# Kernel optimization log

Measured on AMD Instinct MI355X. Metric: run time of the kernel, lower is better.

The kernel has to match this reference:

```python
import jax, jax.numpy as jnp
import numpy as np

NPOINT, NSAMPLE, RADIUS = 2048, 32, 0.2
EPS = 1e-5


def setup_inputs() -> dict:
    key = jax.random.key(0)
    ks = jax.random.split(key, 12)
    B, N, C = 8, 8192, 64
    mlp = [64, 64, 128]
    inp = {
        "xyz": jax.random.normal(ks[0], (B, 3, N), dtype=jnp.float32),
        "points": jax.random.normal(ks[1], (B, C, N), dtype=jnp.float32),
    }
    last = C + 3  # use_xyz concatenates 3 relative coords
    for i, out in enumerate(mlp, 1):
        inp[f"W{i}"] = jax.random.normal(ks[2 * i], (out, last), dtype=jnp.float32) / np.sqrt(last).astype(np.float32)
        inp[f"b{i}"] = jnp.zeros((out,), jnp.float32)
        inp[f"g{i}"] = jnp.ones((out,), jnp.float32)
        inp[f"be{i}"] = jnp.zeros((out,), jnp.float32)
        last = out
    return inp


def fps(xyz_t, npoint):
    """Farthest point sampling. xyz_t: (B,N,3) -> (B,npoint) int32 indices."""
    xyz_t = jax.lax.stop_gradient(xyz_t)  # indices are non-differentiable
    B, N, _ = xyz_t.shape

    def step(carry, _):
        dists, far = carry  # (B,N), (B,)
        cent = jnp.take_along_axis(xyz_t, far[:, None, None], axis=1)  # (B,1,3)
        d = jnp.sum((xyz_t - cent) ** 2, axis=-1)
        dists = jnp.minimum(dists, d)
        nf = jnp.argmax(dists, axis=-1).astype(jnp.int32)
        return (dists, nf), far

    init = (jnp.full((B, N), 1e10, xyz_t.dtype), jnp.zeros((B,), jnp.int32))
    _, idxs = jax.lax.scan(step, init, None, length=npoint)
    return jnp.transpose(idxs)  # (B, npoint)


def ball_query(xyz_t, new_xyz_t, radius, nsample):
    """First-nsample-in-radius neighbor indices, padded with first hit.
    xyz_t (B,N,3), new_xyz_t (B,M,3) -> (B,M,nsample) int32."""
    B, N, _ = xyz_t.shape
    # squared distances via gemm to avoid (B,M,N,3) intermediate
    sq = (jnp.sum(new_xyz_t ** 2, -1)[:, :, None]
          + jnp.sum(xyz_t ** 2, -1)[:, None, :]
          - 2.0 * jnp.einsum('bmd,bnd->bmn', new_xyz_t, xyz_t))  # (B,M,N)
    cand = jnp.where(sq < radius * radius, jnp.arange(N, dtype=jnp.int32), N)
    idx = jnp.sort(cand, axis=-1)[:, :, :nsample]  # first k in-radius by index order
    first = idx[:, :, :1]
    first = jnp.where(first == N, 0, first)  # guard empty groups
    idx = jnp.where(idx == N, first, idx)
    return idx


def group(feat, idx):
    """feat (B,C,N), idx (B,M,k) -> (B,C,M,k) gathered neighbor features."""
    return jnp.take_along_axis(feat[:, :, None, :], idx[:, None, :, :], axis=3)


def conv_bn_relu(x, W, b, g, be):
    """Shared 1x1 Conv2d + BatchNorm2d (batch stats, training mode) + ReLU.
    x: (B,C,M,K) -> (B,O,M,K)."""
    y = jnp.einsum('oc,bcmk->bomk', W, x) + b[None, :, None, None]
    mu = jnp.mean(y, axis=(0, 2, 3), keepdims=True)
    var = jnp.var(y, axis=(0, 2, 3), keepdims=True)
    y = (y - mu) * jax.lax.rsqrt(var + EPS)
    y = y * g[None, :, None, None] + be[None, :, None, None]
    return jax.nn.relu(y)


def reference(xyz, points, W1, b1, g1, be1, W2, b2, g2, be2, W3, b3, g3, be3):
    xyz_t = jnp.transpose(xyz, (0, 2, 1))  # (B,N,3)
    fidx = fps(xyz_t, NPOINT)  # (B,M)
    new_xyz = jnp.take_along_axis(xyz, fidx[:, None, :], axis=2)  # (B,3,M)
    idx = ball_query(xyz_t, jnp.transpose(new_xyz, (0, 2, 1)), RADIUS, NSAMPLE)  # (B,M,K)
    grouped_xyz = group(xyz, idx) - new_xyz[:, :, :, None]  # (B,3,M,K) centered
    grouped_pts = group(points, idx)  # (B,f,M,K)
    x = jnp.concatenate([grouped_xyz, grouped_pts], axis=1)  # (B,f+3,M,K)
    x = conv_bn_relu(x, W1, b1, g1, be1)
    x = conv_bn_relu(x, W2, b2, g2, be2)
    x = conv_bn_relu(x, W3, b3, g3, be3)
    new_points = jnp.max(x, axis=3)  # (B,mlp[-1],M)
    return (new_xyz, new_points)
```

## Files before the change

### kernel.cpp

```cpp
#include <hip/hip_runtime.h>

#define BB 8
#define NN 8192
#define MM 2048
#define KK 32
#define NTOT (BB*MM*KK)

#define WS_PTS_T  0
#define WS_XYZN   4194304
#define WS_IDX    5242880
#define WS_GPART  5767168
#define WS_PARAMS 6291456
#define WS_ZMAX   6292480
#define WS_ZMIN   8389632
#define WS_TOTAL  10486784

typedef float v2f __attribute__((ext_vector_type(2)));

__global__ __launch_bounds__(256) void k_transpose(const float* __restrict__ pts,
                                                   float* __restrict__ pts_t){
  __shared__ float tile[64][65];
  int bid = blockIdx.x;
  int b = bid >> 7;
  int n0 = (bid & 127) << 6;
  int tx = threadIdx.x & 63, ty = threadIdx.x >> 6;
  const float* src = pts + (size_t)b*64*NN;
  #pragma unroll
  for (int c = ty; c < 64; c += 4)
    tile[c][tx] = src[(size_t)c*NN + n0 + tx];
  __syncthreads();
  float* dst = pts_t + ((size_t)b*NN + n0)*64;
  #pragma unroll
  for (int r = ty; r < 64; r += 4)
    dst[(size_t)r*64 + tx] = tile[tx][r];
}

__global__ __launch_bounds__(256) void k_xyzn(const float* __restrict__ xyz,
                                              float4* __restrict__ xyzn){
  #pragma clang fp contract(off)
  int i = blockIdx.x*256 + threadIdx.x;
  int b = i >> 13, n = i & 8191;
  const float* p = xyz + (size_t)b*3*NN;
  float x = p[n], y = p[NN+n], z = p[2*NN+n];
  float nrm = (x*x + y*y) + z*z;
  xyzn[i] = make_float4(x, y, z, nrm);
}

#define FPS_DPP_STEP(ctrl, rmask)                                            \
  {                                                                          \
    unsigned int lo_ = (unsigned int)key, hi_ = (unsigned int)(key >> 32);   \
    unsigned int sl_ = (unsigned int)__builtin_amdgcn_update_dpp(            \
        (int)lo_, (int)lo_, (ctrl), (rmask), 0xf, false);                    \
    unsigned int sh_ = (unsigned int)__builtin_amdgcn_update_dpp(            \
        (int)hi_, (int)hi_, (ctrl), (rmask), 0xf, false);                    \
    unsigned long long ok_ = ((unsigned long long)sh_ << 32) | sl_;          \
    if (ok_ > key) key = ok_;                                                \
  }

__global__ __launch_bounds__(512,1) void k_fps(const float* __restrict__ xyz,
                                               float* __restrict__ out_newxyz){
  #pragma clang fp contract(off)
  __shared__ float4 sp4[NN];
  __shared__ unsigned long long swk[2][8];
  int b = blockIdx.x, tid = threadIdx.x;
  const float* xb = xyz + (size_t)b*3*NN;
  int n0 = tid << 4;
  v2f px[8], py[8], pz[8], dd[8];
  const float4* xb4 = (const float4*)xb;
  #pragma unroll
  for (int q = 0; q < 4; ++q){
    float4 X = xb4[(n0>>2) + q];
    float4 Y = xb4[(NN>>2) + (n0>>2) + q];
    float4 Z = xb4[((2*NN)>>2) + (n0>>2) + q];
    px[2*q]   = (v2f){X.x, X.y}; px[2*q+1] = (v2f){X.z, X.w};
    py[2*q]   = (v2f){Y.x, Y.y}; py[2*q+1] = (v2f){Y.z, Y.w};
    pz[2*q]   = (v2f){Z.x, Z.y}; pz[2*q+1] = (v2f){Z.z, Z.w};
    dd[2*q]   = (v2f){1e10f,1e10f}; dd[2*q+1] = (v2f){1e10f,1e10f};
    sp4[n0+4*q+0] = make_float4(X.x, Y.x, Z.x, 0.f);
    sp4[n0+4*q+1] = make_float4(X.y, Y.y, Z.y, 0.f);
    sp4[n0+4*q+2] = make_float4(X.z, Y.z, Z.z, 0.f);
    sp4[n0+4*q+3] = make_float4(X.w, Y.w, Z.w, 0.f);
  }
  __syncthreads();
  float4 c0 = sp4[0];
  float cx = c0.x, cy = c0.y, cz = c0.z;
  float* ob = out_newxyz + (size_t)b*3*MM;
  int lane = tid & 63, wid = tid >> 6;
  for (int t = 0; t < MM; ++t){
    if (tid == 0){ ob[t] = cx; ob[MM+t] = cy; ob[2*MM+t] = cz; }
    v2f cvx = (v2f){cx,cx}, cvy = (v2f){cy,cy}, cvz = (v2f){cz,cz};
    v2f bv2 = (v2f){-1.f,-1.f};
    #pragma unroll
    for (int g = 0; g < 8; ++g){
      v2f dx = px[g]-cvx, dy = py[g]-cvy, dz = pz[g]-cvz;
      v2f xx = dx*dx, yy = dy*dy, zz = dz*dz;
      v2f s = xx + yy;
      v2f d = s + zz;
      v2f nd = __builtin_elementwise_min(dd[g], d);
      dd[g] = nd;
      bv2 = __builtin_elementwise_max(bv2, nd);
    }
    float bv = fmaxf(bv2.x, bv2.y);
    int bj = 0;
    #pragma unroll
    for (int g = 7; g >= 0; --g){
      if (dd[g].y == bv) bj = 2*g+1;
      if (dd[g].x == bv) bj = 2*g;
    }
    unsigned int n = (unsigned int)(n0 + bj);
    unsigned long long key =
        ((unsigned long long)__float_as_uint(bv) << 32) | (unsigned int)(~n);
    FPS_DPP_STEP(0x111, 0xf)
    FPS_DPP_STEP(0x112, 0xf)
    FPS_DPP_STEP(0x114, 0xf)
    FPS_DPP_STEP(0x118, 0xf)
    FPS_DPP_STEP(0x142, 0xa)
    FPS_DPP_STEP(0x143, 0xc)
    int buf = t & 1;
    if (lane == 63) swk[buf][wid] = key;
    __syncthreads();
    const unsigned long long* kk = swk[buf];
    unsigned long long k0=kk[0], k1=kk[1], k2=kk[2], k3=kk[3];
    unsigned long long k4=kk[4], k5=kk[5], k6=kk[6], k7=kk[7];
    unsigned long long a = (k0>k1)?k0:k1, c = (k2>k3)?k2:k3;
    unsigned long long e = (k4>k5)?k4:k5, f = (k6>k7)?k6:k7;
    unsigned long long g2 = (a>c)?a:c,   h2 = (e>f)?e:f;
    unsigned long long kmax = (g2>h2)?g2:h2;
    int far = (int)(~(unsigned int)kmax) & (NN-1);
    float4 c4 = sp4[far];
    cx = c4.x; cy = c4.y; cz = c4.z;
  }
}

__global__ __launch_bounds__(256) void k_ballq(const float4* __restrict__ xyzn,
                                               const float* __restrict__ newxyz,
                                               int* __restrict__ idx){
  #pragma clang fp contract(off)
  __shared__ unsigned long long s_mask[32][129];
  __shared__ float4 s_c4[32];
  const float R2 = (float)(0.2*0.2);
  int b = blockIdx.x >> 6;
  int m0 = (blockIdx.x & 63) << 5;
  int tid = threadIdx.x, lane = tid & 63, wv = tid >> 6;
  const float* nb = newxyz + (size_t)b*3*MM;
  if (tid < 32){
    int m = m0 + tid;
    float cx = nb[m], cy = nb[MM+m], cz = nb[2*MM+m];
    float cn = (cx*cx + cy*cy) + cz*cz;
    s_c4[tid] = make_float4(cx, cy, cz, cn);
  }
  __syncthreads();
  const float4* src = xyzn + (size_t)b*NN;
  for (int ci = 0; ci < 32; ++ci){
    int ch = ci*4 + wv;
    float4 p = src[ch*64 + lane];
    #pragma unroll 8
    for (int mi = 0; mi < 32; ++mi){
      float4 c = s_c4[mi];
      float dot = (c.x*p.x + c.y*p.y) + c.z*p.z;
      float sq = (c.w + p.w) - 2.0f*dot;
      unsigned long long mk = __ballot(sq < R2);
      if (lane == 0) s_mask[mi][ch] = mk;
    }
  }
  __syncthreads();
  if (tid < 32){
    int m = m0 + tid;
    int* om = idx + ((size_t)(b*MM + m))*KK;
    int filled = 0, first = -1;
    for (int ch = 0; ch < 128 && filled < KK; ++ch){
      unsigned long long mk = s_mask[tid][ch];
      while (mk){
        int bp = __builtin_ctzll(mk);
        mk &= mk - 1;
        int j = ch*64 + bp;
        if (first < 0) first = j;
        om[filled++] = j;
        if (filled == KK) break;
      }
    }
    int pad = (first < 0) ? 0 : first;
    for (int s = filled; s < KK; ++s) om[s] = pad;
  }
}

__device__ __forceinline__ void accum_ch(float4* acc, const float4* w4, int c, float v){
  #pragma unroll
  for (int o4 = 0; o4 < 16; ++o4){
    float4 w = w4[c*16 + o4];
    acc[o4].x = fmaf(w.x, v, acc[o4].x);
    acc[o4].y = fmaf(w.y, v, acc[o4].y);
    acc[o4].z = fmaf(w.z, v, acc[o4].z);
    acc[o4].w = fmaf(w.w, v, acc[o4].w);
  }
}

__device__ __forceinline__ void conv1_pos(float4* acc, const float* s_w1,
    const float* pts_t, const float4* xyzn, const float* nb, int b, int m, int j){
  #pragma unroll
  for (int o4 = 0; o4 < 16; ++o4) acc[o4] = make_float4(0.f,0.f,0.f,0.f);
  float4 P = xyzn[(size_t)b*NN + j];
  float x0 = P.x - nb[m], x1 = P.y - nb[MM+m], x2 = P.z - nb[2*MM+m];
  const float4* w4 = (const float4*)s_w1;
  accum_ch(acc, w4, 0, x0);
  accum_ch(acc, w4, 1, x1);
  accum_ch(acc, w4, 2, x2);
  const float4* pf = (const float4*)(pts_t + ((size_t)b*NN + j)*64);
  #pragma unroll
  for (int c4 = 0; c4 < 16; ++c4){
    float4 v = pf[c4];
    accum_ch(acc, w4, 3+4*c4+0, v.x);
    accum_ch(acc, w4, 3+4*c4+1, v.y);
    accum_ch(acc, w4, 3+4*c4+2, v.z);
    accum_ch(acc, w4, 3+4*c4+3, v.w);
  }
}

__global__ __launch_bounds__(256,1) void k_conv1_stats(const float* __restrict__ pts_t,
    const float4* __restrict__ xyzn, const float* __restrict__ newxyz,
    const int* __restrict__ idx, const float* __restrict__ W1, float* __restrict__ gpart){
  __shared__ float s_w1[67*64];
  __shared__ float s_z[256*68];
  __shared__ float s_part[4*64*2];
  int tid = threadIdx.x;
  for (int i = tid; i < 67*64; i += 256){ int c = i>>6, o = i&63; s_w1[i] = W1[o*67 + c]; }
  __syncthreads();
  int bid = blockIdx.x, b = bid >> 8, m0 = (bid & 255) << 3;
  int m = m0 + (tid >> 5), k = tid & 31;
  int j = idx[((size_t)(b*MM + m))*KK + k];
  const float* nb = newxyz + (size_t)b*3*MM;
  float4 acc[16];
  conv1_pos(acc, s_w1, pts_t, xyzn, nb, b, m, j);
  #pragma unroll
  for (int o4 = 0; o4 < 16; ++o4) *(float4*)&s_z[tid*68 + o4*4] = acc[o4];
  __syncthreads();
  int o = tid & 63, q = tid >> 6;
  float s = 0.f, sq = 0.f;
  for (int p = q*64; p < q*64 + 64; ++p){ float v = s_z[p*68 + o]; s += v; sq = fmaf(v, v, sq); }
  s_part[(q*64+o)*2] = s; s_part[(q*64+o)*2+1] = sq;
  __syncthreads();
  if (tid < 64){
    float S = 0.f, SQ = 0.f;
    #pragma unroll
    for (int qq = 0; qq < 4; ++qq){ S += s_part[(qq*64+tid)*2]; SQ += s_part[(qq*64+tid)*2+1]; }
    gpart[(size_t)tid*2048 + bid] = S;
    gpart[(size_t)(128+tid)*2048 + bid] = SQ;
  }
}

__global__ __launch_bounds__(256) void k_bnfin(const float* __restrict__ gpart,
    const float* __restrict__ g, const float* __restrict__ be, float* __restrict__ params){
  int o = blockIdx.x, t = threadIdx.x;
  double s = 0.0, sq = 0.0;
  for (int i = t; i < 2048; i += 256){
    s  += (double)gpart[(size_t)o*2048 + i];
    sq += (double)gpart[(size_t)(128+o)*2048 + i];
  }
  __shared__ double ds[256], dq[256];
  ds[t] = s; dq[t] = sq; __syncthreads();
  for (int off = 128; off > 0; off >>= 1){
    if (t < off){ ds[t] += ds[t+off]; dq[t] += dq[t+off]; }
    __syncthreads();
  }
  if (t == 0){
    double mu = ds[0] / (double)NTOT;
    double var = dq[0] / (double)NTOT - mu*mu;
    float A = g[o] / sqrtf((float)var + 1e-5f);
    float Cc = be[o] - (float)mu * A;
    params[o] = A; params[128+o] = Cc;
  }
}

__global__ __launch_bounds__(256,1) void k_conv2_stats(const float* __restrict__ pts_t,
    const float4* __restrict__ xyzn, const float* __restrict__ newxyz,
    const int* __restrict__ idx, const float* __restrict__ W1, const float* __restrict__ W2,
    const float* __restrict__ params1, float* __restrict__ gpart){
  __shared__ float s_w1[67*64];
  __shared__ float s_w2[64*64];
  __shared__ float s_p[128];
  __shared__ float s_z[256*68];
  __shared__ float s_part[4*64*2];
  int tid = threadIdx.x;
  for (int i = tid; i < 67*64; i += 256){ int c = i>>6, o = i&63; s_w1[i] = W1[o*67 + c]; }
  for (int i = tid; i < 64*64; i += 256){ int c = i>>6, o = i&63; s_w2[i] = W2[o*64 + c]; }
  if (tid < 64){ s_p[tid] = params1[tid]; s_p[64+tid] = params1[128+tid]; }
  __syncthreads();
  int bid = blockIdx.x, b = bid >> 8, m0 = (bid & 255) << 3;
  int m = m0 + (tid >> 5), k = tid & 31;
  int j = idx[((size_t)(b*MM + m))*KK + k];
  const float* nb = newxyz + (size_t)b*3*MM;
  float4 acc[16];
  conv1_pos(acc, s_w1, pts_t, xyzn, nb, b, m, j);
  float4 h[16];
  #pragma unroll
  for (int o4 = 0; o4 < 16; ++o4){
    float4 z = acc[o4], hh;
    hh.x = fmaxf(fmaf(s_p[4*o4+0], z.x, s_p[64+4*o4+0]), 0.f);
    hh.y = fmaxf(fmaf(s_p[4*o4+1], z.y, s_p[64+4*o4+1]), 0.f);
    hh.z = fmaxf(fmaf(s_p[4*o4+2], z.z, s_p[64+4*o4+2]), 0.f);
    hh.w = fmaxf(fmaf(s_p[4*o4+3], z.w, s_p[64+4*o4+3]), 0.f);
    h[o4] = hh;
  }
  float4 a2[16];
  #pragma unroll
  for (int o4 = 0; o4 < 16; ++o4) a2[o4] = make_float4(0.f,0.f,0.f,0.f);
  const float4* w24 = (const float4*)s_w2;
  #pragma unroll
  for (int c4 = 0; c4 < 16; ++c4){
    accum_ch(a2, w24, 4*c4+0, h[c4].x);
    accum_ch(a2, w24, 4*c4+1, h[c4].y);
    accum_ch(a2, w24, 4*c4+2, h[c4].z);
    accum_ch(a2, w24, 4*c4+3, h[c4].w);
  }
  #pragma unroll
  for (int o4 = 0; o4 < 16; ++o4) *(float4*)&s_z[tid*68 + o4*4] = a2[o4];
  __syncthreads();
  int o = tid & 63, q = tid >> 6;
  float s = 0.f, sq = 0.f;
  for (int p = q*64; p < q*64 + 64; ++p){ float v = s_z[p*68 + o]; s += v; sq = fmaf(v, v, sq); }
  s_part[(q*64+o)*2] = s; s_part[(q*64+o)*2+1] = sq;
  __syncthreads();
  if (tid < 64){
    float S = 0.f, SQ = 0.f;
    #pragma unroll
    for (int qq = 0; qq < 4; ++qq){ S += s_part[(qq*64+tid)*2]; SQ += s_part[(qq*64+tid)*2+1]; }
    gpart[(size_t)tid*2048 + bid] = S;
    gpart[(size_t)(128+tid)*2048 + bid] = SQ;
  }
}

__global__ __launch_bounds__(256,1) void k_conv3(const float* __restrict__ pts_t,
    const float4* __restrict__ xyzn, const float* __restrict__ newxyz,
    const int* __restrict__ idx, const float* __restrict__ W1, const float* __restrict__ W2,
    const float* __restrict__ W3, const float* __restrict__ params1,
    const float* __restrict__ params2, float* __restrict__ gpart,
    float* __restrict__ zmax, float* __restrict__ zmin){
  __shared__ float s_w1[67*64];
  __shared__ float s_w2[64*64];
  __shared__ float s_p[256];
  __shared__ float s_z[256*68];
  __shared__ float s_sm[8*128*2];
  int tid = threadIdx.x;
  for (int i = tid; i < 67*64; i += 256){ int c = i>>6, o = i&63; s_w1[i] = W1[o*67 + c]; }
  for (int i = tid; i < 64*64; i += 256){ int c = i>>6, o = i&63; s_w2[i] = W2[o*64 + c]; }
  if (tid < 64){
    s_p[tid]      = params1[tid];     s_p[64+tid]  = params1[128+tid];
    s_p[128+tid]  = params2[tid];     s_p[192+tid] = params2[128+tid];
  }
  __syncthreads();
  int bid = blockIdx.x, b = bid >> 8, m0 = (bid & 255) << 3;
  {
    int m = m0 + (tid >> 5), k = tid & 31;
    int j = idx[((size_t)(b*MM + m))*KK + k];
    const float* nb = newxyz + (size_t)b*3*MM;
    float4 acc[16];
    conv1_pos(acc, s_w1, pts_t, xyzn, nb, b, m, j);
    float4 h[16];
    #pragma unroll
    for (int o4 = 0; o4 < 16; ++o4){
      float4 z = acc[o4], hh;
      hh.x = fmaxf(fmaf(s_p[4*o4+0], z.x, s_p[64+4*o4+0]), 0.f);
      hh.y = fmaxf(fmaf(s_p[4*o4+1], z.y, s_p[64+4*o4+1]), 0.f);
      hh.z = fmaxf(fmaf(s_p[4*o4+2], z.z, s_p[64+4*o4+2]), 0.f);
      hh.w = fmaxf(fmaf(s_p[4*o4+3], z.w, s_p[64+4*o4+3]), 0.f);
      h[o4] = hh;
    }
    float4 a2[16];
    #pragma unroll
    for (int o4 = 0; o4 < 16; ++o4) a2[o4] = make_float4(0.f,0.f,0.f,0.f);
    const float4* w24 = (const float4*)s_w2;
    #pragma unroll
    for (int c4 = 0; c4 < 16; ++c4){
      accum_ch(a2, w24, 4*c4+0, h[c4].x);
      accum_ch(a2, w24, 4*c4+1, h[c4].y);
      accum_ch(a2, w24, 4*c4+2, h[c4].z);
      accum_ch(a2, w24, 4*c4+3, h[c4].w);
    }
    #pragma unroll
    for (int o4 = 0; o4 < 16; ++o4){
      float4 z = a2[o4], hh;
      hh.x = fmaxf(fmaf(s_p[128+4*o4+0], z.x, s_p[192+4*o4+0]), 0.f);
      hh.y = fmaxf(fmaf(s_p[128+4*o4+1], z.y, s_p[192+4*o4+1]), 0.f);
      hh.z = fmaxf(fmaf(s_p[128+4*o4+2], z.z, s_p[192+4*o4+2]), 0.f);
      hh.w = fmaxf(fmaf(s_p[128+4*o4+3], z.w, s_p[192+4*o4+3]), 0.f);
      *(float4*)&s_z[tid*68 + o4*4] = hh;
    }
  }
  __syncthreads();
  int ml = tid >> 5, og = tid & 31;
  float accK[4][32];
  #pragma unroll
  for (int oo = 0; oo < 4; ++oo)
    #pragma unroll
    for (int k2 = 0; k2 < 32; ++k2) accK[oo][k2] = 0.f;
  const float4* w3g = (const float4*)W3;
  #pragma unroll
  for (int c4 = 0; c4 < 16; ++c4){
    float4 w[4];
    #pragma unroll
    for (int oo = 0; oo < 4; ++oo) w[oo] = w3g[(og*4+oo)*16 + c4];
    #pragma unroll
    for (int k2 = 0; k2 < 32; ++k2){
      float4 hv = *(const float4*)&s_z[(ml*32+k2)*68 + c4*4];
      #pragma unroll
      for (int oo = 0; oo < 4; ++oo){
        accK[oo][k2] = fmaf(w[oo].x, hv.x, accK[oo][k2]);
        accK[oo][k2] = fmaf(w[oo].y, hv.y, accK[oo][k2]);
        accK[oo][k2] = fmaf(w[oo].z, hv.z, accK[oo][k2]);
        accK[oo][k2] = fmaf(w[oo].w, hv.w, accK[oo][k2]);
      }
    }
  }
  int m = m0 + ml;
  #pragma unroll
  for (int oo = 0; oo < 4; ++oo){
    float mx = -3.4e38f, mn = 3.4e38f, s = 0.f, sq = 0.f;
    #pragma unroll
    for (int k2 = 0; k2 < 32; ++k2){
      float v = accK[oo][k2];
      mx = fmaxf(mx, v); mn = fminf(mn, v);
      s += v; sq = fmaf(v, v, sq);
    }
    int o = og*4 + oo;
    zmax[((size_t)(b*128 + o))*MM + m] = mx;
    zmin[((size_t)(b*128 + o))*MM + m] = mn;
    s_sm[(ml*128+o)*2] = s; s_sm[(ml*128+o)*2+1] = sq;
  }
  __syncthreads();
  {
    int o = tid >> 1, st = tid & 1;
    float S = 0.f;
    #pragma unroll
    for (int mm = 0; mm < 8; ++mm) S += s_sm[(mm*128+o)*2 + st];
    gpart[(size_t)(st*128+o)*2048 + bid] = S;
  }
}

__global__ __launch_bounds__(256) void k_out(const float* __restrict__ zmax,
    const float* __restrict__ zmin, const float* __restrict__ params3,
    float* __restrict__ out){
  int i = blockIdx.x*256 + threadIdx.x;
  int o = (i >> 11) & 127;
  float A = params3[o], Cc = params3[128+o];
  float v = (A >= 0.f) ? fmaf(A, zmax[i], Cc) : fmaf(A, zmin[i], Cc);
  out[49152 + i] = fmaxf(v, 0.f);
}

extern "C" void kernel_launch(void* const* d_in, const int* in_sizes, int n_in,
                              void* d_out, int out_size, void* d_ws, size_t ws_size,
                              hipStream_t stream){
  const float* xyz    = (const float*)d_in[0];
  const float* points = (const float*)d_in[1];
  const float* W1  = (const float*)d_in[2];
  const float* g1  = (const float*)d_in[4];
  const float* be1 = (const float*)d_in[5];
  const float* W2  = (const float*)d_in[6];
  const float* g2  = (const float*)d_in[8];
  const float* be2 = (const float*)d_in[9];
  const float* W3  = (const float*)d_in[10];
  const float* g3  = (const float*)d_in[12];
  const float* be3 = (const float*)d_in[13];

  if (ws_size < (size_t)WS_TOTAL * sizeof(float)) return;

  float*  ws     = (float*)d_ws;
  float*  pts_t  = ws + WS_PTS_T;
  float4* xyzn   = (float4*)(ws + WS_XYZN);
  int*    idx    = (int*)(ws + WS_IDX);
  float*  gpart  = ws + WS_GPART;
  float*  params = ws + WS_PARAMS;
  float*  zmax   = ws + WS_ZMAX;
  float*  zmin   = ws + WS_ZMIN;
  float*  out    = (float*)d_out;
  float*  newxyz = out;

  hipLaunchKernelGGL(k_fps,       dim3(8),    dim3(512), 0, stream, xyz, newxyz);
  hipLaunchKernelGGL(k_transpose, dim3(1024), dim3(256), 0, stream, points, pts_t);
  hipLaunchKernelGGL(k_xyzn,      dim3(256),  dim3(256), 0, stream, xyz, xyzn);
  hipLaunchKernelGGL(k_ballq,     dim3(512),  dim3(256), 0, stream, xyzn, newxyz, idx);
  hipLaunchKernelGGL(k_conv1_stats, dim3(2048), dim3(256), 0, stream,
                     pts_t, xyzn, newxyz, idx, W1, gpart);
  hipLaunchKernelGGL(k_bnfin, dim3(64), dim3(256), 0, stream, gpart, g1, be1, params+0);
  hipLaunchKernelGGL(k_conv2_stats, dim3(2048), dim3(256), 0, stream,
                     pts_t, xyzn, newxyz, idx, W1, W2, params+0, gpart);
  hipLaunchKernelGGL(k_bnfin, dim3(64), dim3(256), 0, stream, gpart, g2, be2, params+256);
  hipLaunchKernelGGL(k_conv3, dim3(2048), dim3(256), 0, stream,
                     pts_t, xyzn, newxyz, idx, W1, W2, W3, params+0, params+256,
                     gpart, zmax, zmin);
  hipLaunchKernelGGL(k_bnfin, dim3(128), dim3(256), 0, stream, gpart, g3, be3, params+512);
  hipLaunchKernelGGL(k_out, dim3(8192), dim3(256), 0, stream, zmax, zmin, params+512, out);
}
```

Measured before the change: 3.087 ms.

## Register-tile conv1/conv2 stats kernels and batch FPS centroid output writes

```diff
diff --git a/kernel.cpp b/kernel.cpp
--- a/kernel.cpp
+++ b/kernel.cpp
@@ -86,49 +86,53 @@
   float cx = c0.x, cy = c0.y, cz = c0.z;
   float* ob = out_newxyz + (size_t)b*3*MM;
   int lane = tid & 63, wid = tid >> 6;
-  for (int t = 0; t < MM; ++t){
-    if (tid == 0){ ob[t] = cx; ob[MM+t] = cy; ob[2*MM+t] = cz; }
-    v2f cvx = (v2f){cx,cx}, cvy = (v2f){cy,cy}, cvz = (v2f){cz,cz};
-    v2f bv2 = (v2f){-1.f,-1.f};
-    #pragma unroll
-    for (int g = 0; g < 8; ++g){
-      v2f dx = px[g]-cvx, dy = py[g]-cvy, dz = pz[g]-cvz;
-      v2f xx = dx*dx, yy = dy*dy, zz = dz*dz;
-      v2f s = xx + yy;
-      v2f d = s + zz;
-      v2f nd = __builtin_elementwise_min(dd[g], d);
-      dd[g] = nd;
-      bv2 = __builtin_elementwise_max(bv2, nd);
-    }
-    float bv = fmaxf(bv2.x, bv2.y);
-    int bj = 0;
-    #pragma unroll
-    for (int g = 7; g >= 0; --g){
-      if (dd[g].y == bv) bj = 2*g+1;
-      if (dd[g].x == bv) bj = 2*g;
-    }
-    unsigned int n = (unsigned int)(n0 + bj);
-    unsigned long long key =
-        ((unsigned long long)__float_as_uint(bv) << 32) | (unsigned int)(~n);
-    FPS_DPP_STEP(0x111, 0xf)
-    FPS_DPP_STEP(0x112, 0xf)
-    FPS_DPP_STEP(0x114, 0xf)
-    FPS_DPP_STEP(0x118, 0xf)
-    FPS_DPP_STEP(0x142, 0xa)
-    FPS_DPP_STEP(0x143, 0xc)
-    int buf = t & 1;
-    if (lane == 63) swk[buf][wid] = key;
-    __syncthreads();
-    const unsigned long long* kk = swk[buf];
-    unsigned long long k0=kk[0], k1=kk[1], k2=kk[2], k3=kk[3];
-    unsigned long long k4=kk[4], k5=kk[5], k6=kk[6], k7=kk[7];
-    unsigned long long a = (k0>k1)?k0:k1, c = (k2>k3)?k2:k3;
-    unsigned long long e = (k4>k5)?k4:k5, f = (k6>k7)?k6:k7;
-    unsigned long long g2 = (a>c)?a:c,   h2 = (e>f)?e:f;
-    unsigned long long kmax = (g2>h2)?g2:h2;
-    int far = (int)(~(unsigned int)kmax) & (NN-1);
-    float4 c4 = sp4[far];
-    cx = c4.x; cy = c4.y; cz = c4.z;
+  for (int s = 0; s < 4; ++s){
+    float ox = 0.f, oy = 0.f, oz = 0.f;
+    for (int ti = 0; ti < 512; ++ti){
+      if (tid == ti){ ox = cx; oy = cy; oz = cz; }
+      v2f cvx = (v2f){cx,cx}, cvy = (v2f){cy,cy}, cvz = (v2f){cz,cz};
+      v2f bv2 = (v2f){-1.f,-1.f};
+      #pragma unroll
+      for (int g = 0; g < 8; ++g){
+        v2f dx = px[g]-cvx, dy = py[g]-cvy, dz = pz[g]-cvz;
+        v2f xx = dx*dx, yy = dy*dy, zz = dz*dz;
+        v2f sum = xx + yy;
+        v2f d = sum + zz;
+        v2f nd = __builtin_elementwise_min(dd[g], d);
+        dd[g] = nd;
+        bv2 = __builtin_elementwise_max(bv2, nd);
+      }
+      float bv = fmaxf(bv2.x, bv2.y);
+      int bj = 0;
+      #pragma unroll
+      for (int g = 7; g >= 0; --g){
+        if (dd[g].y == bv) bj = 2*g+1;
+        if (dd[g].x == bv) bj = 2*g;
+      }
+      unsigned int n = (unsigned int)(n0 + bj);
+      unsigned long long key =
+          ((unsigned long long)__float_as_uint(bv) << 32) | (unsigned int)(~n);
+      FPS_DPP_STEP(0x111, 0xf)
+      FPS_DPP_STEP(0x112, 0xf)
+      FPS_DPP_STEP(0x114, 0xf)
+      FPS_DPP_STEP(0x118, 0xf)
+      FPS_DPP_STEP(0x142, 0xa)
+      FPS_DPP_STEP(0x143, 0xc)
+      int buf = ti & 1;
+      if (lane == 63) swk[buf][wid] = key;
+      __syncthreads();
+      const unsigned long long* kk = swk[buf];
+      unsigned long long k0=kk[0], k1=kk[1], k2=kk[2], k3=kk[3];
+      unsigned long long k4=kk[4], k5=kk[5], k6=kk[6], k7=kk[7];
+      unsigned long long a = (k0>k1)?k0:k1, c = (k2>k3)?k2:k3;
+      unsigned long long e = (k4>k5)?k4:k5, f = (k6>k7)?k6:k7;
+      unsigned long long g2 = (a>c)?a:c,   h2 = (e>f)?e:f;
+      unsigned long long kmax = (g2>h2)?g2:h2;
+      int far = (int)(~(unsigned int)kmax) & (NN-1);
+      float4 c4 = sp4[far];
+      cx = c4.x; cy = c4.y; cz = c4.z;
+    }
+    ob[(s<<9)+tid] = ox; ob[MM+(s<<9)+tid] = oy; ob[2*MM+(s<<9)+tid] = oz;
   }
 }
 
@@ -184,6 +188,142 @@
   }
 }
 
+#define XST 260
+
+__device__ __forceinline__ void fma_po(float4& a0, float4& a1, float w,
+                                       const float4& xA, const float4& xB){
+  a0.x = fmaf(w, xA.x, a0.x); a0.y = fmaf(w, xA.y, a0.y);
+  a0.z = fmaf(w, xA.z, a0.z); a0.w = fmaf(w, xA.w, a0.w);
+  a1.x = fmaf(w, xB.x, a1.x); a1.y = fmaf(w, xB.y, a1.y);
+  a1.z = fmaf(w, xB.z, a1.z); a1.w = fmaf(w, xB.w, a1.w);
+}
+
+__device__ __forceinline__ void gemm_step(float4 (&acc)[8][2], const float* sw,
+                                          const float* sx, int c, int ob8, int pb){
+  float4 xA = *(const float4*)&sx[c*XST + pb];
+  float4 xB = *(const float4*)&sx[c*XST + pb + 4];
+  float4 wA = *(const float4*)&sw[c*64 + ob8];
+  float4 wB = *(const float4*)&sw[c*64 + ob8 + 4];
+  fma_po(acc[0][0], acc[0][1], wA.x, xA, xB);
+  fma_po(acc[1][0], acc[1][1], wA.y, xA, xB);
+  fma_po(acc[2][0], acc[2][1], wA.z, xA, xB);
+  fma_po(acc[3][0], acc[3][1], wA.w, xA, xB);
+  fma_po(acc[4][0], acc[4][1], wB.x, xA, xB);
+  fma_po(acc[5][0], acc[5][1], wB.y, xA, xB);
+  fma_po(acc[6][0], acc[6][1], wB.z, xA, xB);
+  fma_po(acc[7][0], acc[7][1], wB.w, xA, xB);
+}
+
+__device__ __forceinline__ void gather_col(float* sx, const float* pts_t,
+    const float4* xyzn, const float* nb, const int* idx, int b, int bid, int tid){
+  int m0 = (bid & 255) << 3;
+  int m = m0 + (tid >> 5), k = tid & 31;
+  int j = idx[((size_t)(b*MM + m))*KK + k];
+  float4 P = xyzn[(size_t)b*NN + j];
+  sx[0*XST + tid] = P.x - nb[m];
+  sx[1*XST + tid] = P.y - nb[MM+m];
+  sx[2*XST + tid] = P.z - nb[2*MM+m];
+  const float4* pf = (const float4*)(pts_t + ((size_t)b*NN + j)*64);
+  #pragma unroll
+  for (int c4 = 0; c4 < 16; ++c4){
+    float4 v = pf[c4];
+    sx[(3+4*c4+0)*XST + tid] = v.x;
+    sx[(3+4*c4+1)*XST + tid] = v.y;
+    sx[(3+4*c4+2)*XST + tid] = v.z;
+    sx[(3+4*c4+3)*XST + tid] = v.w;
+  }
+}
+
+__device__ __forceinline__ void tile_stats(const float4 (&acc)[8][2], float* s_pp,
+    float* gpart, int ob8, int pg, int tid, int bid, int nch_base){
+  #pragma unroll
+  for (int oi = 0; oi < 8; ++oi){
+    float4 a0 = acc[oi][0], a1 = acc[oi][1];
+    float s  = ((a0.x+a0.y)+(a0.z+a0.w)) + ((a1.x+a1.y)+(a1.z+a1.w));
+    float q2 = ((a0.x*a0.x + a0.y*a0.y) + (a0.z*a0.z + a0.w*a0.w))
+             + ((a1.x*a1.x + a1.y*a1.y) + (a1.z*a1.z + a1.w*a1.w));
+    int o = ob8 + oi;
+    s_pp[o*64 + pg*2 + 0] = s;
+    s_pp[o*64 + pg*2 + 1] = q2;
+  }
+  __syncthreads();
+  if (tid < 128){
+    int o = tid >> 1, st = tid & 1;
+    float S = 0.f;
+    #pragma unroll 8
+    for (int q = 0; q < 32; ++q) S += s_pp[o*64 + q*2 + st];
+    gpart[(size_t)(st*128 + nch_base + o)*2048 + bid] = S;
+  }
+}
+
+__global__ __launch_bounds__(256,1) void k_conv1_stats(const float* __restrict__ pts_t,
+    const float4* __restrict__ xyzn, const float* __restrict__ newxyz,
+    const int* __restrict__ idx, const float* __restrict__ W1, float* __restrict__ gpart){
+  __shared__ float s_w1[67*64];
+  __shared__ float s_x[67*XST];
+  int tid = threadIdx.x;
+  for (int i = tid; i < 67*64; i += 256){ int c = i>>6, o = i&63; s_w1[i] = W1[o*67 + c]; }
+  int bid = blockIdx.x, b = bid >> 8;
+  const float* nb = newxyz + (size_t)b*3*MM;
+  gather_col(s_x, pts_t, xyzn, nb, idx, b, bid, tid);
+  __syncthreads();
+  int oq = tid & 7, pg = tid >> 3;
+  int ob8 = oq*8, pb = pg*8;
+  float4 acc[8][2];
+  #pragma unroll
+  for (int oi=0;oi<8;++oi){ acc[oi][0]=make_float4(0,0,0,0); acc[oi][1]=make_float4(0,0,0,0); }
+  for (int c = 0; c < 67; ++c) gemm_step(acc, s_w1, s_x, c, ob8, pb);
+  __syncthreads();
+  tile_stats(acc, s_x, gpart, ob8, pg, tid, bid, 0);
+}
+
+__global__ __launch_bounds__(256,1) void k_conv2_stats(const float* __restrict__ pts_t,
+    const float4* __restrict__ xyzn, const float* __restrict__ newxyz,
+    const int* __restrict__ idx, const float* __restrict__ W1, const float* __restrict__ W2,
+    const float* __restrict__ params1, float* __restrict__ gpart){
+  __shared__ float s_w1[67*64];
+  __shared__ float s_w2[64*64];
+  __shared__ float s_p[128];
+  __shared__ float s_x[67*XST];
+  int tid = threadIdx.x;
+  for (int i = tid; i < 67*64; i += 256){ int c = i>>6, o = i&63; s_w1[i] = W1[o*67 + c]; }
+  for (int i = tid; i < 64*64; i += 256){ int c = i>>6, o = i&63; s_w2[i] = W2[o*64 + c]; }
+  if (tid < 64){ s_p[tid] = params1[tid]; s_p[64+tid] = params1[128+tid]; }
+  int bid = blockIdx.x, b = bid >> 8;
+  const float* nb = newxyz + (size_t)b*3*MM;
+  gather_col(s_x, pts_t, xyzn, nb, idx, b, bid, tid);
+  __syncthreads();
+  int oq = tid & 7, pg = tid >> 3;
+  int ob8 = oq*8, pb = pg*8;
+  float4 acc[8][2];
+  #pragma unroll
+  for (int oi=0;oi<8;++oi){ acc[oi][0]=make_float4(0,0,0,0); acc[oi][1]=make_float4(0,0,0,0); }
+  for (int c = 0; c < 67; ++c) gemm_step(acc, s_w1, s_x, c, ob8, pb);
+  float4 hreg[8][2];
+  #pragma unroll
+  for (int oi = 0; oi < 8; ++oi){
+    float A = s_p[ob8+oi], C = s_p[64+ob8+oi];
+    float4 z0 = acc[oi][0], z1 = acc[oi][1], h0, h1;
+    h0.x = fmaxf(fmaf(A, z0.x, C), 0.f); h0.y = fmaxf(fmaf(A, z0.y, C), 0.f);
+    h0.z = fmaxf(fmaf(A, z0.z, C), 0.f); h0.w = fmaxf(fmaf(A, z0.w, C), 0.f);
+    h1.x = fmaxf(fmaf(A, z1.x, C), 0.f); h1.y = fmaxf(fmaf(A, z1.y, C), 0.f);
+    h1.z = fmaxf(fmaf(A, z1.z, C), 0.f); h1.w = fmaxf(fmaf(A, z1.w, C), 0.f);
+    hreg[oi][0] = h0; hreg[oi][1] = h1;
+  }
+  __syncthreads();
+  #pragma unroll
+  for (int oi = 0; oi < 8; ++oi){
+    *(float4*)&s_x[(ob8+oi)*XST + pb]     = hreg[oi][0];
+    *(float4*)&s_x[(ob8+oi)*XST + pb + 4] = hreg[oi][1];
+  }
+  __syncthreads();
+  #pragma unroll
+  for (int oi=0;oi<8;++oi){ acc[oi][0]=make_float4(0,0,0,0); acc[oi][1]=make_float4(0,0,0,0); }
+  for (int c = 0; c < 64; ++c) gemm_step(acc, s_w2, s_x, c, ob8, pb);
+  __syncthreads();
+  tile_stats(acc, s_x, gpart, ob8, pg, tid, bid, 0);
+}
+
 __device__ __forceinline__ void accum_ch(float4* acc, const float4* w4, int c, float v){
   #pragma unroll
   for (int o4 = 0; o4 < 16; ++o4){
@@ -216,38 +356,6 @@
   }
 }
 
-__global__ __launch_bounds__(256,1) void k_conv1_stats(const float* __restrict__ pts_t,
-    const float4* __restrict__ xyzn, const float* __restrict__ newxyz,
-    const int* __restrict__ idx, const float* __restrict__ W1, float* __restrict__ gpart){
-  __shared__ float s_w1[67*64];
-  __shared__ float s_z[256*68];
-  __shared__ float s_part[4*64*2];
-  int tid = threadIdx.x;
-  for (int i = tid; i < 67*64; i += 256){ int c = i>>6, o = i&63; s_w1[i] = W1[o*67 + c]; }
-  __syncthreads();
-  int bid = blockIdx.x, b = bid >> 8, m0 = (bid & 255) << 3;
-  int m = m0 + (tid >> 5), k = tid & 31;
-  int j = idx[((size_t)(b*MM + m))*KK + k];
-  const float* nb = newxyz + (size_t)b*3*MM;
-  float4 acc[16];
-  conv1_pos(acc, s_w1, pts_t, xyzn, nb, b, m, j);
-  #pragma unroll
-  for (int o4 = 0; o4 < 16; ++o4) *(float4*)&s_z[tid*68 + o4*4] = acc[o4];
-  __syncthreads();
-  int o = tid & 63, q = tid >> 6;
-  float s = 0.f, sq = 0.f;
-  for (int p = q*64; p < q*64 + 64; ++p){ float v = s_z[p*68 + o]; s += v; sq = fmaf(v, v, sq); }
-  s_part[(q*64+o)*2] = s; s_part[(q*64+o)*2+1] = sq;
-  __syncthreads();
-  if (tid < 64){
-    float S = 0.f, SQ = 0.f;
-    #pragma unroll
-    for (int qq = 0; qq < 4; ++qq){ S += s_part[(qq*64+tid)*2]; SQ += s_part[(qq*64+tid)*2+1]; }
-    gpart[(size_t)tid*2048 + bid] = S;
-    gpart[(size_t)(128+tid)*2048 + bid] = SQ;
-  }
-}
-
 __global__ __launch_bounds__(256) void k_bnfin(const float* __restrict__ gpart,
     const float* __restrict__ g, const float* __restrict__ be, float* __restrict__ params){
   int o = blockIdx.x, t = threadIdx.x;
@@ -268,64 +376,6 @@
     float A = g[o] / sqrtf((float)var + 1e-5f);
     float Cc = be[o] - (float)mu * A;
     params[o] = A; params[128+o] = Cc;
-  }
-}
-
-__global__ __launch_bounds__(256,1) void k_conv2_stats(const float* __restrict__ pts_t,
-    const float4* __restrict__ xyzn, const float* __restrict__ newxyz,
-    const int* __restrict__ idx, const float* __restrict__ W1, const float* __restrict__ W2,
-    const float* __restrict__ params1, float* __restrict__ gpart){
-  __shared__ float s_w1[67*64];
-  __shared__ float s_w2[64*64];
-  __shared__ float s_p[128];
-  __shared__ float s_z[256*68];
-  __shared__ float s_part[4*64*2];
-  int tid = threadIdx.x;
-  for (int i = tid; i < 67*64; i += 256){ int c = i>>6, o = i&63; s_w1[i] = W1[o*67 + c]; }
-  for (int i = tid; i < 64*64; i += 256){ int c = i>>6, o = i&63; s_w2[i] = W2[o*64 + c]; }
-  if (tid < 64){ s_p[tid] = params1[tid]; s_p[64+tid] = params1[128+tid]; }
-  __syncthreads();
-  int bid = blockIdx.x, b = bid >> 8, m0 = (bid & 255) << 3;
-  int m = m0 + (tid >> 5), k = tid & 31;
-  int j = idx[((size_t)(b*MM + m))*KK + k];
-  const float* nb = newxyz + (size_t)b*3*MM;
-  float4 acc[16];
-  conv1_pos(acc, s_w1, pts_t, xyzn, nb, b, m, j);
-  float4 h[16];
-  #pragma unroll
-  for (int o4 = 0; o4 < 16; ++o4){
-    float4 z = acc[o4], hh;
-    hh.x = fmaxf(fmaf(s_p[4*o4+0], z.x, s_p[64+4*o4+0]), 0.f);
-    hh.y = fmaxf(fmaf(s_p[4*o4+1], z.y, s_p[64+4*o4+1]), 0.f);
-    hh.z = fmaxf(fmaf(s_p[4*o4+2], z.z, s_p[64+4*o4+2]), 0.f);
-    hh.w = fmaxf(fmaf(s_p[4*o4+3], z.w, s_p[64+4*o4+3]), 0.f);
-    h[o4] = hh;
-  }
-  float4 a2[16];
-  #pragma unroll
-  for (int o4 = 0; o4 < 16; ++o4) a2[o4] = make_float4(0.f,0.f,0.f,0.f);
-  const float4* w24 = (const float4*)s_w2;
-  #pragma unroll
-  for (int c4 = 0; c4 < 16; ++c4){
-    accum_ch(a2, w24, 4*c4+0, h[c4].x);
-    accum_ch(a2, w24, 4*c4+1, h[c4].y);
-    accum_ch(a2, w24, 4*c4+2, h[c4].z);
-    accum_ch(a2, w24, 4*c4+3, h[c4].w);
-  }
-  #pragma unroll
-  for (int o4 = 0; o4 < 16; ++o4) *(float4*)&s_z[tid*68 + o4*4] = a2[o4];
-  __syncthreads();
-  int o = tid & 63, q = tid >> 6;
-  float s = 0.f, sq = 0.f;
-  for (int p = q*64; p < q*64 + 64; ++p){ float v = s_z[p*68 + o]; s += v; sq = fmaf(v, v, sq); }
-  s_part[(q*64+o)*2] = s; s_part[(q*64+o)*2+1] = sq;
-  __syncthreads();
-  if (tid < 64){
-    float S = 0.f, SQ = 0.f;
-    #pragma unroll
-    for (int qq = 0; qq < 4; ++qq){ S += s_part[(qq*64+tid)*2]; SQ += s_part[(qq*64+tid)*2+1]; }
-    gpart[(size_t)tid*2048 + bid] = S;
-    gpart[(size_t)(128+tid)*2048 + bid] = SQ;
   }
 }
 
```

Result: faster. 2.895 ms (-6.2%).
